# Kernel optimization log

Hardware: AMD Instinct MI355X
Metric: run time of the kernel (lower is better)

## Reference

```python
import jax, jax.numpy as jnp
import numpy as np

B = 1; H = 256; W = 256; C = 192; HEADS = 6; WS = 16; SHIFT = 8
N = WS * WS; HD = C // HEADS; HID = 4 * C


def setup_inputs() -> dict:
    key = jax.random.key(0)
    ks = jax.random.split(key, 8)
    # relative position index (standard Swin construction)
    coords = np.stack(np.meshgrid(np.arange(WS), np.arange(WS), indexing='ij'))  # 2,ws,ws
    cf = coords.reshape(2, -1)
    rel = (cf[:, :, None] - cf[:, None, :]).transpose(1, 2, 0)  # n,n,2
    rel[..., 0] += WS - 1
    rel[..., 1] += WS - 1
    rel[..., 0] *= 2 * WS - 1
    rpi = rel.sum(-1).astype(np.int32)  # [N,N], values in [0, (2*WS-1)^2)
    # shifted-window attention mask (standard Swin construction)
    img = np.zeros((1, H, W, 1), np.float32)
    cnt = 0
    sl = (slice(0, -WS), slice(-WS, -SHIFT), slice(-SHIFT, None))
    for hs in sl:
        for ws_ in sl:
            img[:, hs, ws_, :] = cnt
            cnt += 1
    mw = img.reshape(1, H // WS, WS, W // WS, WS, 1).transpose(0, 1, 3, 2, 4, 5).reshape(-1, N)
    diff = mw[:, None, :] - mw[:, :, None]  # [nw, N, N]
    attn_mask = np.where(diff != 0, np.float32(-100.0), np.float32(0.0))
    std = 0.02
    p = lambda k, shp: jax.random.normal(k, shp, jnp.float32) * std
    return {
        'x': jax.random.normal(ks[0], (B, H * W, C), jnp.float32),
        'rpi_sa': jnp.asarray(rpi),
        'attn_mask': jnp.asarray(attn_mask),
        'norm1_g': jnp.ones((C,), jnp.float32), 'norm1_b': jnp.zeros((C,), jnp.float32),
        'qkv_w': p(ks[1], (C, 3 * C)), 'qkv_b': jnp.zeros((3 * C,), jnp.float32),
        'rpb_table': p(ks[2], ((2 * WS - 1) * (2 * WS - 1), HEADS)),
        'proj_w': p(ks[3], (C, C)), 'proj_b': jnp.zeros((C,), jnp.float32),
        'norm2_g': jnp.ones((C,), jnp.float32), 'norm2_b': jnp.zeros((C,), jnp.float32),
        'fc1_w': p(ks[4], (C, HID)), 'fc1_b': jnp.zeros((HID,), jnp.float32),
        'fc2_w': p(ks[5], (HID, C)), 'fc2_b': jnp.zeros((C,), jnp.float32),
    }


def _ln(x, g, b):
    m = x.mean(-1, keepdims=True)
    v = ((x - m) ** 2).mean(-1, keepdims=True)
    return (x - m) * jax.lax.rsqrt(v + 1e-5) * g + b


def reference(x, rpi_sa, attn_mask, norm1_g, norm1_b, qkv_w, qkv_b, rpb_table,
              proj_w, proj_b, norm2_g, norm2_b, fc1_w, fc1_b, fc2_w, fc2_b):
    b = x.shape[0]
    shortcut = x
    h = _ln(x, norm1_g, norm1_b).reshape(b, H, W, C)
    h = jnp.roll(h, (-SHIFT, -SHIFT), axis=(1, 2))
    # window partition -> (b*nw, N, C)
    xw = h.reshape(b, H // WS, WS, W // WS, WS, C).transpose(0, 1, 3, 2, 4, 5).reshape(-1, N, C)
    qkv = (xw @ qkv_w + qkv_b).reshape(-1, N, 3, HEADS, HD).transpose(2, 0, 3, 1, 4)
    q, k, v = qkv[0] * (HD ** -0.5), qkv[1], qkv[2]  # [b_, H, N, HD]
    attn = jnp.einsum('bhnd,bhmd->bhnm', q, k)  # [b_, H, N, N]
    bias = rpb_table[rpi_sa.reshape(-1)].reshape(N, N, HEADS).transpose(2, 0, 1)
    attn = attn + bias[None]
    nw = attn_mask.shape[0]
    attn = attn.reshape(-1, nw, HEADS, N, N) + attn_mask[None, :, None]
    attn = jax.nn.softmax(attn.reshape(-1, HEADS, N, N), axis=-1)
    out = jnp.einsum('bhnm,bhmd->bnhd', attn, v).reshape(-1, N, C)
    out = out @ proj_w + proj_b
    # window reverse + unshift
    out = out.reshape(b, H // WS, W // WS, WS, WS, C).transpose(0, 1, 3, 2, 4, 5).reshape(b, H, W, C)
    out = jnp.roll(out, (SHIFT, SHIFT), axis=(1, 2)).reshape(b, H * W, C)
    xr = shortcut + out  # drop_path = identity (eval / drop_prob=0)
    y = _ln(xr, norm2_g, norm2_b)
    y = jax.nn.gelu(y @ fc1_w + fc1_b, approximate=False) @ fc2_w + fc2_b
    return xr + y
```

## Files before the change

kernel.cpp:

```cpp
#include <hip/hip_runtime.h>
#include <math.h>

#define NHEADS 6
#define CC 192
#define HDIM 32
#define NTOK 256
#define SHIFTV 8

typedef __attribute__((ext_vector_type(8))) short short8;
typedef __attribute__((ext_vector_type(4))) short short4v;
typedef __attribute__((ext_vector_type(4))) float floatx4;

__device__ inline short f2bf(float f) {
    union { float f; unsigned u; } v; v.f = f;
    unsigned r = (v.u + 0x7FFFu + ((v.u >> 16) & 1u)) >> 16;
    return (short)r;
}

__device__ inline float gelu_f(float x) {
    float x2 = x * x;
    float p = x * (-1.5957691216f - 0.07135481627f * x2);
    float e = __expf(p);
    return x * __builtin_amdgcn_rcpf(1.f + e);
}

__global__ __launch_bounds__(256) void bias_kernel(const int* __restrict__ rpi,
                                                   const float* __restrict__ rpb,
                                                   float* __restrict__ biasB) {
    int idx = blockIdx.x * 256 + threadIdx.x;
    int m = idx & 255;
    int n = (idx >> 8) & 255;
    int h = idx >> 16;
    biasB[idx] = rpb[rpi[n * 256 + m] * NHEADS + h];
}

__global__ __launch_bounds__(256) void cvt_kernel(const float* __restrict__ qkvw,
                                                  const float* __restrict__ pw,
                                                  const float* __restrict__ f1w,
                                                  const float* __restrict__ f2w,
                                                  short* __restrict__ wqt,
                                                  short* __restrict__ pwt,
                                                  short* __restrict__ w1t,
                                                  short* __restrict__ w2t) {
    int idx = blockIdx.x * 256 + threadIdx.x;
    int n = idx / 192, k = idx - n * 192;
    w1t[idx] = f2bf(f1w[k * 768 + n]);
    int c = idx / 768, h = idx - c * 768;
    w2t[idx] = f2bf(f2w[h * 192 + c]);
    if (idx < 576 * 192) wqt[idx] = f2bf(qkvw[k * 576 + n]);
    if (idx < 192 * 192) pwt[idx] = f2bf(pw[k * 192 + n]);
}

__global__ __launch_bounds__(256) void qkv_kernel(const float* __restrict__ x,
        const float* __restrict__ g1, const float* __restrict__ b1,
        const short* __restrict__ wqt, const float* __restrict__ qkvb,
        ushort* __restrict__ Qb, ushort* __restrict__ Kb, ushort* __restrict__ VTb) {
    __shared__ __align__(16) short xln[64 * 200];
    __shared__ float red[64][4][2];
    const int t = threadIdx.x;
    const int g0 = blockIdx.x * 64;
    const int w = g0 >> 8;
    {
        int row = t >> 2, part = t & 3;
        int n = (g0 + row) & 255;
        int sy = (((w >> 4) << 4) + (n >> 4) + SHIFTV) & 255;
        int sx = (((w & 15) << 4) + (n & 15) + SHIFTV) & 255;
        const float* xr = x + (sy * 256 + sx) * CC + part * 48;
        float vals[48];
        float s = 0.f, ss = 0.f;
        #pragma unroll
        for (int i = 0; i < 48; ++i) { float v = xr[i]; vals[i] = v; s += v; ss += v * v; }
        red[row][part][0] = s; red[row][part][1] = ss;
        __syncthreads();
        float sum = red[row][0][0] + red[row][1][0] + red[row][2][0] + red[row][3][0];
        float sq  = red[row][0][1] + red[row][1][1] + red[row][2][1] + red[row][3][1];
        float mean = sum * (1.f / 192.f);
        float var = sq * (1.f / 192.f) - mean * mean;
        float inv = rsqrtf(var + 1e-5f);
        #pragma unroll
        for (int i = 0; i < 48; ++i) {
            int c = part * 48 + i;
            xln[row * 200 + c] = f2bf((vals[i] - mean) * inv * g1[c] + b1[c]);
        }
    }
    __syncthreads();
    const int wv = t >> 6, lane = t & 63;
    const int lr = lane & 15;
    const int lk = (lane >> 4) * 8;
    const int q4 = (lane >> 4) * 4;
    #pragma unroll
    for (int jc = 0; jc < 3; ++jc) {
        floatx4 acc[4][3];
        #pragma unroll
        for (int mt = 0; mt < 4; ++mt)
            #pragma unroll
            for (int nt = 0; nt < 3; ++nt) acc[mt][nt] = floatx4{0.f,0.f,0.f,0.f};
        for (int ks = 0; ks < 6; ++ks) {
            int k0 = ks * 32 + lk;
            short8 a[4];
            #pragma unroll
            for (int mt = 0; mt < 4; ++mt)
                a[mt] = *(const short8*)&xln[(mt * 16 + lr) * 200 + k0];
            #pragma unroll
            for (int nt = 0; nt < 3; ++nt) {
                int nglob = jc * 192 + wv * 48 + nt * 16 + lr;
                short8 b = *(const short8*)&wqt[nglob * 192 + k0];
                #pragma unroll
                for (int mt = 0; mt < 4; ++mt)
                    acc[mt][nt] = __builtin_amdgcn_mfma_f32_16x16x32_bf16(a[mt], b, acc[mt][nt], 0, 0, 0);
            }
        }
        #pragma unroll
        for (int nt = 0; nt < 3; ++nt) {
            int jj = wv * 48 + nt * 16 + lr;
            float bias = qkvb[jc * 192 + jj];
            int head = jj >> 5, hd = jj & 31;
            int wh = w * NHEADS + head;
            #pragma unroll
            for (int mt = 0; mt < 4; ++mt) {
                int nr0 = (g0 + mt * 16 + q4) & 255;
                if (jc == 0) {
                    #pragma unroll
                    for (int reg = 0; reg < 4; ++reg)
                        Qb[((size_t)wh * NTOK + nr0 + reg) * HDIM + hd] =
                            (ushort)f2bf((acc[mt][nt][reg] + bias) * 0.17677669529663687f);
                } else if (jc == 1) {
                    #pragma unroll
                    for (int reg = 0; reg < 4; ++reg)
                        Kb[((size_t)wh * NTOK + nr0 + reg) * HDIM + hd] =
                            (ushort)f2bf(acc[mt][nt][reg] + bias);
                } else {
                    short4v pk;
                    #pragma unroll
                    for (int reg = 0; reg < 4; ++reg)
                        pk[reg] = f2bf(acc[mt][nt][reg] + bias);
                    *(short4v*)&VTb[((size_t)wh * HDIM + hd) * NTOK + nr0] = pk;
                }
            }
        }
    }
}

__global__ __launch_bounds__(256) void attn_kernel(const ushort* __restrict__ Q,
        const ushort* __restrict__ K, const ushort* __restrict__ VT,
        const float* __restrict__ biasB,
        ushort* __restrict__ Ob) {
    __shared__ __align__(16) ushort Ks[256 * 40];
    __shared__ __align__(16) ushort Vs[32 * 264];
    __shared__ __align__(16) ushort Ps[4][64 * 40];
    const int t = threadIdx.x;
    const int wh = blockIdx.x;
    const int w = wh / 6, h = wh - w * 6;
    const int wy = w >> 4, wx = w & 15;
    {
        const ushort* kg = K + (size_t)wh * (NTOK * HDIM);
        const ushort* vg = VT + (size_t)wh * (NTOK * HDIM);
        for (int i = t * 8; i < NTOK * HDIM; i += 2048) {
            short8 kv = *(const short8*)(kg + i);
            *(short8*)&Ks[(i >> 5) * 40 + (i & 31)] = kv;
            short8 vv = *(const short8*)(vg + i);
            *(short8*)&Vs[(i >> 8) * 264 + (i & 255)] = vv;
        }
    }
    const int wv = t >> 6, lane = t & 63;
    const int lc = lane & 15;
    const int q4 = (lane >> 4) * 4;
    const int lk8 = (lane >> 4) * 8;
    const int qb = wv * 64;
    const bool cmask = (wx == 15) && ((lc >= 8) != (q4 >= 8));
    const bool rowY  = (wy == 15);
    short8 qf[4];
    {
        const ushort* qg = Q + (size_t)wh * (NTOK * HDIM);
        #pragma unroll
        for (int qt = 0; qt < 4; ++qt)
            qf[qt] = *(const short8*)(qg + (qb + qt * 16 + lc) * HDIM + lk8);
    }
    __syncthreads();
    float Ssum[4];
    floatx4 o[2][4];
    #pragma unroll
    for (int qt = 0; qt < 4; ++qt) {
        Ssum[qt] = 0.f;
        o[0][qt] = floatx4{0.f,0.f,0.f,0.f};
        o[1][qt] = floatx4{0.f,0.f,0.f,0.f};
    }
    ushort* Pw = &Ps[wv][0];
    const float* bp = biasB + h * 65536;
    for (int kc = 0; kc < 8; ++kc) {
        const int k0 = kc * 32;
        short8 ka[2];
        ka[0] = *(const short8*)&Ks[(k0 + lc) * 40 + lk8];
        ka[1] = *(const short8*)&Ks[(k0 + 16 + lc) * 40 + lk8];
        floatx4 sf[2][4];
        #pragma unroll
        for (int kt = 0; kt < 2; ++kt)
            #pragma unroll
            for (int qt = 0; qt < 4; ++qt)
                sf[kt][qt] = __builtin_amdgcn_mfma_f32_16x16x32_bf16(ka[kt], qf[qt],
                                floatx4{0.f,0.f,0.f,0.f}, 0, 0, 0);
        #pragma unroll
        for (int kt = 0; kt < 2; ++kt)
            #pragma unroll
            for (int qt = 0; qt < 4; ++qt) {
                int q = qb + qt * 16 + lc;
                int kbase = k0 + kt * 16 + q4;
                bool msk = cmask || (rowY && (((wv * 4 + qt) >= 8) != ((kc * 2 + kt) >= 8)));
                float4 bb = *(const float4*)(bp + q * 256 + kbase);
                float p0 = msk ? 0.f : __expf(sf[kt][qt][0] + bb.x);
                float p1 = msk ? 0.f : __expf(sf[kt][qt][1] + bb.y);
                float p2 = msk ? 0.f : __expf(sf[kt][qt][2] + bb.z);
                float p3 = msk ? 0.f : __expf(sf[kt][qt][3] + bb.w);
                Ssum[qt] += (p0 + p1) + (p2 + p3);
                short4v pk;
                pk.x = f2bf(p0); pk.y = f2bf(p1); pk.z = f2bf(p2); pk.w = f2bf(p3);
                *(short4v*)&Pw[(qt * 16 + lc) * 40 + kt * 16 + q4] = pk;
            }
        short8 va[2], pf[4];
        va[0] = *(const short8*)&Vs[lc * 264 + k0 + lk8];
        va[1] = *(const short8*)&Vs[(16 + lc) * 264 + k0 + lk8];
        #pragma unroll
        for (int qt = 0; qt < 4; ++qt)
            pf[qt] = *(const short8*)&Pw[(qt * 16 + lc) * 40 + lk8];
        #pragma unroll
        for (int ht = 0; ht < 2; ++ht)
            #pragma unroll
            for (int qt = 0; qt < 4; ++qt)
                o[ht][qt] = __builtin_amdgcn_mfma_f32_16x16x32_bf16(va[ht], pf[qt], o[ht][qt], 0, 0, 0);
    }
    #pragma unroll
    for (int qt = 0; qt < 4; ++qt) {
        float rs = Ssum[qt];
        rs += __shfl_xor(rs, 16);
        rs += __shfl_xor(rs, 32);
        float inv = 1.f / rs;
        size_t rowbase = ((size_t)(w * NTOK + qb + qt * 16 + lc)) * CC + h * HDIM;
        #pragma unroll
        for (int ht = 0; ht < 2; ++ht)
            #pragma unroll
            for (int r = 0; r < 4; ++r)
                Ob[rowbase + ht * 16 + q4 + r] = (ushort)f2bf(o[ht][qt][r] * inv);
    }
}

__global__ __launch_bounds__(256) void proj_kernel(const ushort* __restrict__ Ob,
        const short* __restrict__ pwt, const float* __restrict__ pb,
        const float* __restrict__ x, float* __restrict__ out) {
    __shared__ __align__(16) short oln[64 * 200];
    const int t = threadIdx.x;
    const int g0 = blockIdx.x * 64;
    const int w = g0 >> 8;
    {
        int row = t >> 2, part = t & 3;
        const ushort* orow = Ob + (size_t)(g0 + row) * CC + part * 48;
        #pragma unroll
        for (int i = 0; i < 6; ++i)
            *(short8*)&oln[row * 200 + part * 48 + i * 8] = *(const short8*)(orow + i * 8);
    }
    __syncthreads();
    const int wv = t >> 6, lane = t & 63;
    const int lr = lane & 15;
    const int lk = (lane >> 4) * 8;
    const int q4 = (lane >> 4) * 4;
    floatx4 acc[4][3];
    #pragma unroll
    for (int mt = 0; mt < 4; ++mt)
        #pragma unroll
        for (int nt = 0; nt < 3; ++nt) acc[mt][nt] = floatx4{0.f,0.f,0.f,0.f};
    for (int ks = 0; ks < 6; ++ks) {
        int k0 = ks * 32 + lk;
        short8 a[4];
        #pragma unroll
        for (int mt = 0; mt < 4; ++mt)
            a[mt] = *(const short8*)&oln[(mt * 16 + lr) * 200 + k0];
        #pragma unroll
        for (int nt = 0; nt < 3; ++nt) {
            int c = wv * 48 + nt * 16 + lr;
            short8 b = *(const short8*)&pwt[c * 192 + k0];
            #pragma unroll
            for (int mt = 0; mt < 4; ++mt)
                acc[mt][nt] = __builtin_amdgcn_mfma_f32_16x16x32_bf16(a[mt], b, acc[mt][nt], 0, 0, 0);
        }
    }
    #pragma unroll
    for (int nt = 0; nt < 3; ++nt) {
        int c = wv * 48 + nt * 16 + lr;
        float bias = pb[c];
        #pragma unroll
        for (int mt = 0; mt < 4; ++mt) {
            #pragma unroll
            for (int reg = 0; reg < 4; ++reg) {
                int nn = (g0 + mt * 16 + q4 + reg) & 255;
                int sy = (((w >> 4) << 4) + (nn >> 4) + SHIFTV) & 255;
                int sx = (((w & 15) << 4) + (nn & 15) + SHIFTV) & 255;
                size_t base = (size_t)(sy * 256 + sx) * CC;
                out[base + c] = x[base + c] + acc[mt][nt][reg] + bias;
            }
        }
    }
}

__global__ __launch_bounds__(256) void mlp_kernel(const float* __restrict__ g2,
        const float* __restrict__ b2, const short* __restrict__ w1t,
        const float* __restrict__ f1b, const short* __restrict__ w2t,
        const float* __restrict__ f2b, float* __restrict__ out) {
    __shared__ __align__(16) short xln[64 * 200];
    __shared__ __align__(16) short Hs[64 * 200];
    __shared__ float red[64][4][2];
    const int t = threadIdx.x;
    const int m0 = blockIdx.x * 64;
    {
        int row = t >> 2, part = t & 3;
        const float* xr = out + (size_t)(m0 + row) * CC + part * 48;
        float vals[48];
        float s = 0.f, ss = 0.f;
        #pragma unroll
        for (int i = 0; i < 48; ++i) { float v = xr[i]; vals[i] = v; s += v; ss += v * v; }
        red[row][part][0] = s; red[row][part][1] = ss;
        __syncthreads();
        float sum = red[row][0][0] + red[row][1][0] + red[row][2][0] + red[row][3][0];
        float sq  = red[row][0][1] + red[row][1][1] + red[row][2][1] + red[row][3][1];
        float mean = sum * (1.f / 192.f);
        float var = sq * (1.f / 192.f) - mean * mean;
        float inv = rsqrtf(var + 1e-5f);
        #pragma unroll
        for (int i = 0; i < 48; ++i) {
            int c = part * 48 + i;
            xln[row * 200 + c] = f2bf((vals[i] - mean) * inv * g2[c] + b2[c]);
        }
    }
    __syncthreads();
    const int wv = t >> 6;
    const int lane = t & 63;
    const int lr = lane & 15;
    const int lk = (lane >> 4) * 8;
    const int q4 = (lane >> 4) * 4;
    floatx4 acc2[4][3];
    #pragma unroll
    for (int mt = 0; mt < 4; ++mt)
        #pragma unroll
        for (int nt = 0; nt < 3; ++nt) acc2[mt][nt] = floatx4{0.f, 0.f, 0.f, 0.f};

    for (int hc = 0; hc < 4; ++hc) {
        floatx4 acc1[4][3];
        #pragma unroll
        for (int mt = 0; mt < 4; ++mt)
            #pragma unroll
            for (int nt = 0; nt < 3; ++nt) acc1[mt][nt] = floatx4{0.f, 0.f, 0.f, 0.f};
        for (int ks = 0; ks < 6; ++ks) {
            int k0 = ks * 32 + lk;
            short8 a[4];
            #pragma unroll
            for (int mt = 0; mt < 4; ++mt)
                a[mt] = *(const short8*)&xln[(mt * 16 + lr) * 200 + k0];
            #pragma unroll
            for (int nt = 0; nt < 3; ++nt) {
                int n = hc * 192 + wv * 48 + nt * 16 + lr;
                short8 b = *(const short8*)&w1t[n * 192 + k0];
                #pragma unroll
                for (int mt = 0; mt < 4; ++mt)
                    acc1[mt][nt] = __builtin_amdgcn_mfma_f32_16x16x32_bf16(a[mt], b, acc1[mt][nt], 0, 0, 0);
            }
        }
        __syncthreads();
        #pragma unroll
        for (int nt = 0; nt < 3; ++nt) {
            int colb = wv * 48 + nt * 16 + lr;
            float bias = f1b[hc * 192 + colb];
            #pragma unroll
            for (int mt = 0; mt < 4; ++mt) {
                #pragma unroll
                for (int reg = 0; reg < 4; ++reg) {
                    float v = acc1[mt][nt][reg] + bias;
                    Hs[(mt * 16 + q4 + reg) * 200 + colb] = f2bf(gelu_f(v));
                }
            }
        }
        __syncthreads();
        for (int ks = 0; ks < 6; ++ks) {
            int k0 = ks * 32 + lk;
            short8 a[4];
            #pragma unroll
            for (int mt = 0; mt < 4; ++mt)
                a[mt] = *(const short8*)&Hs[(mt * 16 + lr) * 200 + k0];
            #pragma unroll
            for (int nt = 0; nt < 3; ++nt) {
                int c = wv * 48 + nt * 16 + lr;
                short8 b = *(const short8*)&w2t[c * 768 + hc * 192 + k0];
                #pragma unroll
                for (int mt = 0; mt < 4; ++mt)
                    acc2[mt][nt] = __builtin_amdgcn_mfma_f32_16x16x32_bf16(a[mt], b, acc2[mt][nt], 0, 0, 0);
            }
        }
    }
    #pragma unroll
    for (int nt = 0; nt < 3; ++nt) {
        int c = wv * 48 + nt * 16 + lr;
        float bias = f2b[c];
        #pragma unroll
        for (int mt = 0; mt < 4; ++mt) {
            #pragma unroll
            for (int reg = 0; reg < 4; ++reg) {
                size_t off = (size_t)(m0 + mt * 16 + q4 + reg) * CC + c;
                out[off] = out[off] + acc2[mt][nt][reg] + bias;
            }
        }
    }
}

extern "C" void kernel_launch(void* const* d_in, const int* in_sizes, int n_in,
                              void* d_out, int out_size, void* d_ws, size_t ws_size,
                              hipStream_t stream) {
    (void)in_sizes; (void)n_in; (void)out_size; (void)ws_size;
    const float* x    = (const float*)d_in[0];
    const int*   rpi  = (const int*)d_in[1];
    const float* n1g  = (const float*)d_in[3];
    const float* n1b  = (const float*)d_in[4];
    const float* qkvw = (const float*)d_in[5];
    const float* qkvb = (const float*)d_in[6];
    const float* rpb  = (const float*)d_in[7];
    const float* pw   = (const float*)d_in[8];
    const float* pb   = (const float*)d_in[9];
    const float* n2g  = (const float*)d_in[10];
    const float* n2b  = (const float*)d_in[11];
    const float* f1w  = (const float*)d_in[12];
    const float* f1b  = (const float*)d_in[13];
    const float* f2w  = (const float*)d_in[14];
    const float* f2b  = (const float*)d_in[15];
    float* out = (float*)d_out;

    ushort* Qb  = (ushort*)d_ws;
    ushort* Kb  = Qb + 12582912;
    ushort* VTb = Kb + 12582912;
    ushort* Ob  = VTb + 12582912;
    float* BIAS = (float*)(Ob + 12582912);
    short* WQT  = (short*)(BIAS + 393216);
    short* PWT  = WQT + 110592;
    short* W1T  = PWT + 36864;
    short* W2T  = W1T + 147456;

    bias_kernel<<<1536, 256, 0, stream>>>(rpi, rpb, BIAS);
    cvt_kernel<<<576, 256, 0, stream>>>(qkvw, pw, f1w, f2w, WQT, PWT, W1T, W2T);
    qkv_kernel<<<1024, 256, 0, stream>>>(x, n1g, n1b, WQT, qkvb, Qb, Kb, VTb);
    attn_kernel<<<1536, 256, 0, stream>>>(Qb, Kb, VTb, BIAS, Ob);
    proj_kernel<<<1024, 256, 0, stream>>>(Ob, PWT, pb, x, out);
    mlp_kernel<<<1024, 256, 0, stream>>>(n2g, n2b, W1T, f1b, W2T, f2b, out);
}
```

Baseline: 455.8 us.

## Fuse projection and MLP kernels, keeping residual in registers

Merges the attention output projection and the MLP into one kernel. The residual sum stays in registers, and LayerNorm2 statistics are computed with wave shuffles plus a small shared reduction instead of re-reading the intermediate from global memory. This removes one full fp32 write and read of the activation tensor and one kernel launch. It raises register pressure because the residual values are held through both MLP GEMMs, which may reduce occupancy.

```diff
diff --git a/kernel.cpp b/kernel.cpp
--- a/kernel.cpp
+++ b/kernel.cpp
@@ -243,10 +243,16 @@
     }
 }
 
-__global__ __launch_bounds__(256) void proj_kernel(const ushort* __restrict__ Ob,
+__global__ __launch_bounds__(256) void projmlp_kernel(const ushort* __restrict__ Ob,
         const short* __restrict__ pwt, const float* __restrict__ pb,
-        const float* __restrict__ x, float* __restrict__ out) {
-    __shared__ __align__(16) short oln[64 * 200];
+        const float* __restrict__ x,
+        const float* __restrict__ g2, const float* __restrict__ b2,
+        const short* __restrict__ w1t, const float* __restrict__ f1b,
+        const short* __restrict__ w2t, const float* __restrict__ f2b,
+        float* __restrict__ out) {
+    __shared__ __align__(16) short olnhs[64 * 200];
+    __shared__ __align__(16) short xln[64 * 200];
+    __shared__ float red[64][4][2];
     const int t = threadIdx.x;
     const int g0 = blockIdx.x * 64;
     const int w = g0 >> 8;
@@ -255,33 +261,34 @@
         const ushort* orow = Ob + (size_t)(g0 + row) * CC + part * 48;
         #pragma unroll
         for (int i = 0; i < 6; ++i)
-            *(short8*)&oln[row * 200 + part * 48 + i * 8] = *(const short8*)(orow + i * 8);
+            *(short8*)&olnhs[row * 200 + part * 48 + i * 8] = *(const short8*)(orow + i * 8);
     }
     __syncthreads();
     const int wv = t >> 6, lane = t & 63;
     const int lr = lane & 15;
     const int lk = (lane >> 4) * 8;
     const int q4 = (lane >> 4) * 4;
-    floatx4 acc[4][3];
+    floatx4 accp[4][3];
     #pragma unroll
     for (int mt = 0; mt < 4; ++mt)
         #pragma unroll
-        for (int nt = 0; nt < 3; ++nt) acc[mt][nt] = floatx4{0.f,0.f,0.f,0.f};
+        for (int nt = 0; nt < 3; ++nt) accp[mt][nt] = floatx4{0.f,0.f,0.f,0.f};
     for (int ks = 0; ks < 6; ++ks) {
         int k0 = ks * 32 + lk;
         short8 a[4];
         #pragma unroll
         for (int mt = 0; mt < 4; ++mt)
-            a[mt] = *(const short8*)&oln[(mt * 16 + lr) * 200 + k0];
+            a[mt] = *(const short8*)&olnhs[(mt * 16 + lr) * 200 + k0];
         #pragma unroll
         for (int nt = 0; nt < 3; ++nt) {
             int c = wv * 48 + nt * 16 + lr;
             short8 b = *(const short8*)&pwt[c * 192 + k0];
             #pragma unroll
             for (int mt = 0; mt < 4; ++mt)
-                acc[mt][nt] = __builtin_amdgcn_mfma_f32_16x16x32_bf16(a[mt], b, acc[mt][nt], 0, 0, 0);
-        }
-    }
+                accp[mt][nt] = __builtin_amdgcn_mfma_f32_16x16x32_bf16(a[mt], b, accp[mt][nt], 0, 0, 0);
+        }
+    }
+    float xr[4][3][4];
     #pragma unroll
     for (int nt = 0; nt < 3; ++nt) {
         int c = wv * 48 + nt * 16 + lr;
@@ -293,54 +300,71 @@
                 int nn = (g0 + mt * 16 + q4 + reg) & 255;
                 int sy = (((w >> 4) << 4) + (nn >> 4) + SHIFTV) & 255;
                 int sx = (((w & 15) << 4) + (nn & 15) + SHIFTV) & 255;
-                size_t base = (size_t)(sy * 256 + sx) * CC;
-                out[base + c] = x[base + c] + acc[mt][nt][reg] + bias;
-            }
-        }
-    }
-}
-
-__global__ __launch_bounds__(256) void mlp_kernel(const float* __restrict__ g2,
-        const float* __restrict__ b2, const short* __restrict__ w1t,
-        const float* __restrict__ f1b, const short* __restrict__ w2t,
-        const float* __restrict__ f2b, float* __restrict__ out) {
-    __shared__ __align__(16) short xln[64 * 200];
-    __shared__ __align__(16) short Hs[64 * 200];
-    __shared__ float red[64][4][2];
-    const int t = threadIdx.x;
-    const int m0 = blockIdx.x * 64;
-    {
-        int row = t >> 2, part = t & 3;
-        const float* xr = out + (size_t)(m0 + row) * CC + part * 48;
-        float vals[48];
-        float s = 0.f, ss = 0.f;
-        #pragma unroll
-        for (int i = 0; i < 48; ++i) { float v = xr[i]; vals[i] = v; s += v; ss += v * v; }
-        red[row][part][0] = s; red[row][part][1] = ss;
-        __syncthreads();
-        float sum = red[row][0][0] + red[row][1][0] + red[row][2][0] + red[row][3][0];
-        float sq  = red[row][0][1] + red[row][1][1] + red[row][2][1] + red[row][3][1];
-        float mean = sum * (1.f / 192.f);
-        float var = sq * (1.f / 192.f) - mean * mean;
-        float inv = rsqrtf(var + 1e-5f);
-        #pragma unroll
-        for (int i = 0; i < 48; ++i) {
-            int c = part * 48 + i;
-            xln[row * 200 + c] = f2bf((vals[i] - mean) * inv * g2[c] + b2[c]);
-        }
+                xr[mt][nt][reg] = x[(size_t)(sy * 256 + sx) * CC + c] + accp[mt][nt][reg] + bias;
+            }
+        }
+    }
+    float sm[4][4], sq[4][4];
+    #pragma unroll
+    for (int mt = 0; mt < 4; ++mt)
+        #pragma unroll
+        for (int reg = 0; reg < 4; ++reg) {
+            float a0 = xr[mt][0][reg], a1 = xr[mt][1][reg], a2 = xr[mt][2][reg];
+            sm[mt][reg] = a0 + a1 + a2;
+            sq[mt][reg] = a0 * a0 + a1 * a1 + a2 * a2;
+        }
+    #pragma unroll
+    for (int msk = 1; msk <= 8; msk <<= 1) {
+        #pragma unroll
+        for (int mt = 0; mt < 4; ++mt)
+            #pragma unroll
+            for (int reg = 0; reg < 4; ++reg) {
+                sm[mt][reg] += __shfl_xor(sm[mt][reg], msk);
+                sq[mt][reg] += __shfl_xor(sq[mt][reg], msk);
+            }
+    }
+    if (lr == 0) {
+        #pragma unroll
+        for (int mt = 0; mt < 4; ++mt)
+            #pragma unroll
+            for (int reg = 0; reg < 4; ++reg) {
+                int r = mt * 16 + q4 + reg;
+                red[r][wv][0] = sm[mt][reg];
+                red[r][wv][1] = sq[mt][reg];
+            }
     }
     __syncthreads();
-    const int wv = t >> 6;
-    const int lane = t & 63;
-    const int lr = lane & 15;
-    const int lk = (lane >> 4) * 8;
-    const int q4 = (lane >> 4) * 4;
+    float mean[4][4], inv[4][4];
+    #pragma unroll
+    for (int mt = 0; mt < 4; ++mt)
+        #pragma unroll
+        for (int reg = 0; reg < 4; ++reg) {
+            int r = mt * 16 + q4 + reg;
+            float s  = red[r][0][0] + red[r][1][0] + red[r][2][0] + red[r][3][0];
+            float ss = red[r][0][1] + red[r][1][1] + red[r][2][1] + red[r][3][1];
+            float m_ = s * (1.f / 192.f);
+            float v_ = ss * (1.f / 192.f) - m_ * m_;
+            mean[mt][reg] = m_;
+            inv[mt][reg] = rsqrtf(v_ + 1e-5f);
+        }
+    #pragma unroll
+    for (int nt = 0; nt < 3; ++nt) {
+        int c = wv * 48 + nt * 16 + lr;
+        float gg = g2[c], bb = b2[c];
+        #pragma unroll
+        for (int mt = 0; mt < 4; ++mt)
+            #pragma unroll
+            for (int reg = 0; reg < 4; ++reg)
+                xln[(mt * 16 + q4 + reg) * 200 + c] =
+                    f2bf((xr[mt][nt][reg] - mean[mt][reg]) * inv[mt][reg] * gg + bb);
+    }
+    __syncthreads();
+    short* Hs = olnhs;
     floatx4 acc2[4][3];
     #pragma unroll
     for (int mt = 0; mt < 4; ++mt)
         #pragma unroll
         for (int nt = 0; nt < 3; ++nt) acc2[mt][nt] = floatx4{0.f, 0.f, 0.f, 0.f};
-
     for (int hc = 0; hc < 4; ++hc) {
         floatx4 acc1[4][3];
         #pragma unroll
@@ -401,8 +425,11 @@
         for (int mt = 0; mt < 4; ++mt) {
             #pragma unroll
             for (int reg = 0; reg < 4; ++reg) {
-                size_t off = (size_t)(m0 + mt * 16 + q4 + reg) * CC + c;
-                out[off] = out[off] + acc2[mt][nt][reg] + bias;
+                int nn = (g0 + mt * 16 + q4 + reg) & 255;
+                int sy = (((w >> 4) << 4) + (nn >> 4) + SHIFTV) & 255;
+                int sx = (((w & 15) << 4) + (nn & 15) + SHIFTV) & 255;
+                out[(size_t)(sy * 256 + sx) * CC + c] =
+                    xr[mt][nt][reg] + acc2[mt][nt][reg] + bias;
             }
         }
     }
@@ -443,6 +470,5 @@
     cvt_kernel<<<576, 256, 0, stream>>>(qkvw, pw, f1w, f2w, WQT, PWT, W1T, W2T);
     qkv_kernel<<<1024, 256, 0, stream>>>(x, n1g, n1b, WQT, qkvb, Qb, Kb, VTb);
     attn_kernel<<<1536, 256, 0, stream>>>(Qb, Kb, VTb, BIAS, Ob);
-    proj_kernel<<<1024, 256, 0, stream>>>(Ob, PWT, pb, x, out);
-    mlp_kernel<<<1024, 256, 0, stream>>>(n2g, n2b, W1T, f1b, W2T, f2b, out);
-}
+    projmlp_kernel<<<1024, 256, 0, stream>>>(Ob, PWT, pb, x, n2g, n2b, W1T, f1b, W2T, f2b, out);
+}
```

New measurement: 456.8 us. No clear change (+0.2%).
